# Kernel optimization log

Hardware: AMD Instinct MI355X
Metric: run time of the kernel (lower is better)

The kernel has to match this reference:

```python
import math
import jax, jax.numpy as jnp
import numpy as np

N = 8192
D_IN = 512
D_E = 512


def setup_inputs() -> dict:
    key = jax.random.key(0)
    k1, k2, k3, k4 = jax.random.split(key, 4)
    x = jax.random.normal(k1, (N, D_IN), dtype=jnp.float32)
    A = jax.random.uniform(k2, (N, N), dtype=jnp.float32)
    # xavier-uniform-ish scaling for the two projection weights
    lim_qkv = math.sqrt(6.0 / (D_IN + 3 * D_E))
    Wqkv = jax.random.uniform(k3, (D_IN, 3 * D_E), dtype=jnp.float32, minval=-lim_qkv, maxval=lim_qkv)
    bqkv = jnp.zeros((3 * D_E,), dtype=jnp.float32)
    lim_o = math.sqrt(6.0 / (D_E + D_E))
    Wo = jax.random.uniform(k4, (D_E, D_E), dtype=jnp.float32, minval=-lim_o, maxval=lim_o)
    bo = jnp.zeros((D_E,), dtype=jnp.float32)
    return {"x": x, "A": A, "Wqkv": Wqkv, "bqkv": bqkv, "Wo": Wo, "bo": bo}


def reference(x, A, Wqkv, bqkv, Wo, bo):
    # qkv projection: [N, 3*D_E]
    qkv = x @ Wqkv + bqkv
    q, k, v = jnp.split(qkv, 3, axis=-1)  # each [N, D_E]
    # graph-adjacency transform of keys
    k = A @ k  # [N, D_E]
    scale = 1.0 / math.sqrt(q.shape[-1])
    attn_logits = (q @ k.T) * scale  # [N, N]
    attention = jax.nn.softmax(attn_logits, axis=-1)
    values = attention @ v  # [N, D_E]
    o = values @ Wo + bo
    return (o, attention)
```

## Files before the change

### kernel.cpp

```cpp
#include <hip/hip_runtime.h>

typedef _Float16 half8 __attribute__((ext_vector_type(8)));
typedef _Float16 half4 __attribute__((ext_vector_type(4)));
typedef float f32x4 __attribute__((ext_vector_type(4)));

__global__ __launch_bounds__(256) void transpose_f32(
    const float* __restrict__ in, int lda,
    float* __restrict__ out, int ldo)
{
  __shared__ float t[32][33];
  const int tx = threadIdx.x & 31, ty = threadIdx.x >> 5;
  const int bc = blockIdx.x * 32, br = blockIdx.y * 32;
#pragma unroll
  for (int i = 0; i < 4; ++i)
    t[ty + 8 * i][tx] = in[(size_t)(br + ty + 8 * i) * lda + bc + tx];
  __syncthreads();
#pragma unroll
  for (int i = 0; i < 4; ++i)
    out[(size_t)(bc + ty + 8 * i) * ldo + br + tx] = t[tx][ty + 8 * i];
}

__global__ __launch_bounds__(256) void transpose_f32_f16(
    const float* __restrict__ in, int lda,
    _Float16* __restrict__ out, int ldo)
{
  __shared__ float t[32][33];
  const int tx = threadIdx.x & 31, ty = threadIdx.x >> 5;
  const int bc = blockIdx.x * 32, br = blockIdx.y * 32;
#pragma unroll
  for (int i = 0; i < 4; ++i)
    t[ty + 8 * i][tx] = in[(size_t)(br + ty + 8 * i) * lda + bc + tx];
  __syncthreads();
#pragma unroll
  for (int i = 0; i < 4; ++i)
    out[(size_t)(bc + ty + 8 * i) * ldo + br + tx] = (_Float16)t[tx][ty + 8 * i];
}

__global__ __launch_bounds__(256) void conv_f32_f16(
    const float4* __restrict__ in, _Float16* __restrict__ out)
{
  size_t i = (size_t)blockIdx.x * 256 + threadIdx.x;
  float4 v = in[i];
  half4 h;
  h[0] = (_Float16)v.x; h[1] = (_Float16)v.y;
  h[2] = (_Float16)v.z; h[3] = (_Float16)v.w;
  ((half4*)out)[i] = h;
}

__global__ __launch_bounds__(256) void halfcolsum16(
    const _Float16* __restrict__ k0T16, float* __restrict__ csum)
{
  const int d = blockIdx.x, tid = threadIdx.x;
  float s = 0.f;
#pragma unroll
  for (int i = 0; i < 4; ++i) {
    half8 h = *(const half8*)(k0T16 + (size_t)d * 8192 + i * 2048 + tid * 8);
#pragma unroll
    for (int j = 0; j < 8; ++j) s += (float)h[j];
  }
#pragma unroll
  for (int off = 32; off; off >>= 1) s += __shfl_xor(s, off);
  __shared__ float r[4];
  if ((tid & 63) == 0) r[tid >> 6] = s;
  __syncthreads();
  if (tid == 0) csum[d] = 0.5f * ((r[0] + r[1]) + (r[2] + r[3]));
}

template<int ASPL,int BSPL,int BM,int BN,int WAVES_M,int WAVES_N,int THREADS,
         int APART,bool KSPLIT,bool QF16,int MINW,int AMODE,int BMODE>
__global__ __launch_bounds__(THREADS, MINW) void gemm_bt(
    const void* __restrict__ Agv, int lda, size_t a_plane,
    const void* __restrict__ Bgv, int ldb, size_t b_plane,
    float* __restrict__ Cg, int ldc, size_t c_plane,
    const float* __restrict__ bias, int K, float scale,
    _Float16* __restrict__ q16out)
{
  constexpr int BK = 32;
  constexpr int WM = BM / WAVES_M, WN = BN / WAVES_N;
  constexpr int FM = WM / 16, FN = WN / 16;
  constexpr int NCA = (BM * 4) / THREADS;
  constexpr int NCB = (BN * 4) / THREADS;
  static_assert((BM * 4) % THREADS == 0 && (BN * 4) % THREADS == 0, "mismatch");
  static_assert(AMODE != 3 || ASPL == 1, "AMODE 3 needs ASPL 1");

  __shared__ _Float16 ldsA[2][ASPL][BM][BK];
  __shared__ _Float16 ldsB[2][BSPL][BN][BK];

  const float*    Ag   = (const float*)Agv;
  const _Float16* Ag16 = (const _Float16*)Agv;
  const float*    Bg   = (const float*)Bgv;
  const _Float16* Bg16 = (const _Float16*)Bgv;

  const int tid  = threadIdx.x;
  const int lane = tid & 63;
  const int wid  = tid >> 6;
  const int wrow = wid / WAVES_N, wcol = wid % WAVES_N;
  const int l15  = lane & 15, g = lane >> 4;
  const int brow = blockIdx.y * BM;
  const int bcol = blockIdx.x * BN;

  if constexpr (KSPLIT) {
    const int kc = blockIdx.z;
    Ag += (size_t)kc * K;  Ag16 += (size_t)kc * K;
    Bg += (size_t)kc * K;  Bg16 += (size_t)kc * K;
    Cg += (size_t)kc * c_plane;
  }

  f32x4 acc[FM][FN];
#pragma unroll
  for (int mi = 0; mi < FM; ++mi)
#pragma unroll
    for (int ni = 0; ni < FN; ++ni)
      acc[mi][ni] = (f32x4){0.f, 0.f, 0.f, 0.f};

  float4 ra[NCA][2], rb[NCB][2];
  half8  rah[NCA][2], rbh[NCB][2];

  auto loadAB = [&](int kt) {
    const int k0 = kt * BK;
#pragma unroll
    for (int i = 0; i < NCA; ++i) {
      int c = tid + THREADS * i;
      int row = c >> 2, ci = c & 3;
      if constexpr (AMODE == 3) {
        rah[i][0] = *(const half8*)(Ag16 + (size_t)(brow + row) * lda + k0 + ci * 8);
      } else if constexpr (AMODE == 2) {
        const _Float16* bp = Ag16 + (size_t)(brow + row) * lda + k0 + ci * 8;
        rah[i][0] = *(const half8*)bp;
        rah[i][1] = *(const half8*)(bp + a_plane);
      } else if constexpr (AMODE == 1) {
        float4 u0 = make_float4(0.f, 0.f, 0.f, 0.f);
        float4 u1 = make_float4(0.f, 0.f, 0.f, 0.f);
        const _Float16* bp = Ag16 + (size_t)(brow + row) * lda + k0 + ci * 8;
#pragma unroll
        for (int p = 0; p < APART; ++p) {
          half8 hv = *(const half8*)(bp + (size_t)p * a_plane);
          u0.x += (float)hv[0]; u0.y += (float)hv[1]; u0.z += (float)hv[2]; u0.w += (float)hv[3];
          u1.x += (float)hv[4]; u1.y += (float)hv[5]; u1.z += (float)hv[6]; u1.w += (float)hv[7];
        }
        ra[i][0] = u0; ra[i][1] = u1;
      } else {
        const float* bp = Ag + (size_t)(brow + row) * lda + k0 + ci * 8;
        float4 u0 = ((const float4*)bp)[0];
        float4 u1 = ((const float4*)bp)[1];
#pragma unroll
        for (int p = 1; p < APART; ++p) {
          const float* pp = bp + (size_t)p * a_plane;
          float4 w0 = ((const float4*)pp)[0], w1 = ((const float4*)pp)[1];
          u0.x += w0.x; u0.y += w0.y; u0.z += w0.z; u0.w += w0.w;
          u1.x += w1.x; u1.y += w1.y; u1.z += w1.z; u1.w += w1.w;
        }
        ra[i][0] = u0; ra[i][1] = u1;
      }
    }
#pragma unroll
    for (int i = 0; i < NCB; ++i) {
      int c = tid + THREADS * i;
      int row = c >> 2, ci = c & 3;
      if constexpr (BMODE == 2) {
        const _Float16* bp = Bg16 + (size_t)(bcol + row) * ldb + k0 + ci * 8;
        rbh[i][0] = *(const half8*)bp;
        rbh[i][1] = *(const half8*)(bp + b_plane);
      } else if constexpr (BMODE == 3) {
        rbh[i][0] = *(const half8*)(Bg16 + (size_t)(bcol + row) * ldb + k0 + ci * 8);
      } else {
        const float4* p = (const float4*)(Bg + (size_t)(bcol + row) * ldb + k0 + ci * 8);
        rb[i][0] = p[0]; rb[i][1] = p[1];
      }
    }
  };

  auto stageLDS = [&](int b) {
#pragma unroll
    for (int i = 0; i < NCA; ++i) {
      int c = tid + THREADS * i;
      int row = c >> 2, ci = c & 3;
      int off = row * BK + ((ci ^ ((row >> 1) & 3)) << 3);
      if constexpr (AMODE == 3) {
        *(half8*)(&ldsA[b][0][0][0] + off) = rah[i][0];
      } else if constexpr (AMODE == 2) {
        *(half8*)(&ldsA[b][0][0][0] + off) = rah[i][0];
        *(half8*)(&ldsA[b][1][0][0] + off) = rah[i][1];
      } else {
        float f[8] = {ra[i][0].x, ra[i][0].y, ra[i][0].z, ra[i][0].w,
                      ra[i][1].x, ra[i][1].y, ra[i][1].z, ra[i][1].w};
        half8 h, l;
#pragma unroll
        for (int j = 0; j < 8; ++j) {
          _Float16 hv = (_Float16)f[j];
          h[j] = hv;
          if (ASPL == 2) l[j] = (_Float16)(f[j] - (float)hv);
        }
        *(half8*)(&ldsA[b][0][0][0] + off) = h;
        if (ASPL == 2) *(half8*)(&ldsA[b][1][0][0] + off) = l;
      }
    }
#pragma unroll
    for (int i = 0; i < NCB; ++i) {
      int c = tid + THREADS * i;
      int row = c >> 2, ci = c & 3;
      int off = row * BK + ((ci ^ ((row >> 1) & 3)) << 3);
      if constexpr (BMODE == 2) {
        *(half8*)(&ldsB[b][0][0][0] + off) = rbh[i][0];
        *(half8*)(&ldsB[b][1][0][0] + off) = rbh[i][1];
      } else if constexpr (BMODE == 3) {
        *(half8*)(&ldsB[b][0][0][0] + off) = rbh[i][0];
      } else {
        float f[8] = {rb[i][0].x, rb[i][0].y, rb[i][0].z, rb[i][0].w,
                      rb[i][1].x, rb[i][1].y, rb[i][1].z, rb[i][1].w};
        half8 h, l;
#pragma unroll
        for (int j = 0; j < 8; ++j) {
          _Float16 hv = (_Float16)f[j];
          h[j] = hv;
          if (BSPL == 2) l[j] = (_Float16)(f[j] - (float)hv);
        }
        *(half8*)(&ldsB[b][0][0][0] + off) = h;
        if (BSPL == 2) *(half8*)(&ldsB[b][1][0][0] + off) = l;
      }
    }
  };

  const int nk = K / BK;
  loadAB(0);
  stageLDS(0);
  if (nk > 1) loadAB(1);
  __syncthreads();

  for (int kt = 0; kt < nk; ++kt) {
    const int cur = kt & 1, nxt = cur ^ 1;
    if (kt + 1 < nk) stageLDS(nxt);
    if (kt + 2 < nk) loadAB(kt + 2);

    half8 af[FM][ASPL];
#pragma unroll
    for (int mi = 0; mi < FM; ++mi)
#pragma unroll
      for (int sa = 0; sa < ASPL; ++sa) {
        int row = wrow * WM + mi * 16 + l15;
        af[mi][sa] = *(const half8*)(&ldsA[cur][sa][0][0] + row * BK + ((g ^ ((row >> 1) & 3)) << 3));
      }
#pragma unroll
    for (int ni = 0; ni < FN; ++ni) {
      half8 bf[BSPL];
#pragma unroll
      for (int sb = 0; sb < BSPL; ++sb) {
        int row = wcol * WN + ni * 16 + l15;
        bf[sb] = *(const half8*)(&ldsB[cur][sb][0][0] + row * BK + ((g ^ ((row >> 1) & 3)) << 3));
      }
#pragma unroll
      for (int mi = 0; mi < FM; ++mi)
#pragma unroll
        for (int sa = 0; sa < ASPL; ++sa)
#pragma unroll
          for (int sb = 0; sb < BSPL; ++sb) {
            if (ASPL == 2 && BSPL == 2 && sa == 1 && sb == 1) continue;
            acc[mi][ni] = __builtin_amdgcn_mfma_f32_16x16x32_f16(af[mi][sa], bf[sb], acc[mi][ni], 0, 0, 0);
          }
    }
    __syncthreads();
  }

#pragma unroll
  for (int mi = 0; mi < FM; ++mi)
#pragma unroll
    for (int ni = 0; ni < FN; ++ni) {
      int col = bcol + wcol * WN + ni * 16 + l15;
      float bv = bias ? bias[col] : 0.f;
#pragma unroll
      for (int j = 0; j < 4; ++j) {
        int r = brow + wrow * WM + mi * 16 + g * 4 + j;
        float v = acc[mi][ni][j] * scale + bv;
        if constexpr (QF16) {
          if (col < 512) q16out[(size_t)r * 512 + col] = (_Float16)v;
          else           Cg[(size_t)r * ldc + col] = v;
        } else {
          Cg[(size_t)r * ldc + col] = v;
        }
      }
    }
}

template<int BM,int BN,int THREADS,bool STATS,int MINW>
__global__ __launch_bounds__(THREADS, MINW) void gemm_ff16(
    const _Float16* __restrict__ Ag, int lda,
    const _Float16* __restrict__ Bg, int ldb,
    float* __restrict__ Cg, int ldc,
    int K, float scale,
    float* __restrict__ mxout, float* __restrict__ smout, int ntiles)
{
  constexpr int BK = 32;
  constexpr int WAVES_M = 2, WAVES_N = 2;
  constexpr int WM = BM / WAVES_M, WN = BN / WAVES_N;
  constexpr int FM = WM / 16, FN = WN / 16;
  constexpr int NCA = (BM * 4) / THREADS;
  constexpr int NCB = (BN * 4) / THREADS;

  __shared__ _Float16 ldsA[2][BM][BK];
  __shared__ _Float16 ldsB[2][BN][BK];

  const int tid  = threadIdx.x;
  const int lane = tid & 63;
  const int wid  = tid >> 6;
  const int wrow = wid >> 1, wcol = wid & 1;
  const int l15  = lane & 15, g = lane >> 4;
  const int brow = blockIdx.y * BM;
  const int bcol = blockIdx.x * BN;

  f32x4 acc[FM][FN];
#pragma unroll
  for (int mi = 0; mi < FM; ++mi)
#pragma unroll
    for (int ni = 0; ni < FN; ++ni)
      acc[mi][ni] = (f32x4){0.f, 0.f, 0.f, 0.f};

  half8 ra[NCA], rb[NCB];

  auto loadAB = [&](int kt) {
    const int k0 = kt * BK;
#pragma unroll
    for (int i = 0; i < NCA; ++i) {
      int c = tid + THREADS * i;
      int row = c >> 2, ci = c & 3;
      ra[i] = *(const half8*)(Ag + (size_t)(brow + row) * lda + k0 + ci * 8);
    }
#pragma unroll
    for (int i = 0; i < NCB; ++i) {
      int c = tid + THREADS * i;
      int row = c >> 2, ci = c & 3;
      rb[i] = *(const half8*)(Bg + (size_t)(bcol + row) * ldb + k0 + ci * 8);
    }
  };

  auto stageLDS = [&](int b) {
#pragma unroll
    for (int i = 0; i < NCA; ++i) {
      int c = tid + THREADS * i;
      int row = c >> 2, ci = c & 3;
      int off = row * BK + ((ci ^ ((row >> 1) & 3)) << 3);
      *(half8*)(&ldsA[b][0][0] + off) = ra[i];
    }
#pragma unroll
    for (int i = 0; i < NCB; ++i) {
      int c = tid + THREADS * i;
      int row = c >> 2, ci = c & 3;
      int off = row * BK + ((ci ^ ((row >> 1) & 3)) << 3);
      *(half8*)(&ldsB[b][0][0] + off) = rb[i];
    }
  };

  const int nk = K / BK;
  loadAB(0);
  stageLDS(0);
  if (nk > 1) loadAB(1);
  __syncthreads();

  for (int kt = 0; kt < nk; ++kt) {
    const int cur = kt & 1, nxt = cur ^ 1;
    if (kt + 1 < nk) stageLDS(nxt);
    if (kt + 2 < nk) loadAB(kt + 2);

    half8 af[FM];
#pragma unroll
    for (int mi = 0; mi < FM; ++mi) {
      int row = wrow * WM + mi * 16 + l15;
      af[mi] = *(const half8*)(&ldsA[cur][0][0] + row * BK + ((g ^ ((row >> 1) & 3)) << 3));
    }
#pragma unroll
    for (int ni = 0; ni < FN; ++ni) {
      int row = wcol * WN + ni * 16 + l15;
      half8 bf = *(const half8*)(&ldsB[cur][0][0] + row * BK + ((g ^ ((row >> 1) & 3)) << 3));
#pragma unroll
      for (int mi = 0; mi < FM; ++mi)
        acc[mi][ni] = __builtin_amdgcn_mfma_f32_16x16x32_f16(af[mi], bf, acc[mi][ni], 0, 0, 0);
    }
    __syncthreads();
  }

#pragma unroll
  for (int mi = 0; mi < FM; ++mi)
#pragma unroll
    for (int ni = 0; ni < FN; ++ni) {
      int col = bcol + wcol * WN + ni * 16 + l15;
#pragma unroll
      for (int j = 0; j < 4; ++j) {
        int r = brow + wrow * WM + mi * 16 + g * 4 + j;
        Cg[(size_t)r * ldc + col] = acc[mi][ni][j] * scale;
      }
    }

  if constexpr (STATS) {
    __shared__ float s_m2[BM][2];
    __shared__ float s_s2[BM][2];
#pragma unroll
    for (int mi = 0; mi < FM; ++mi)
#pragma unroll
      for (int j = 0; j < 4; ++j) {
        float v = -3.4e38f;
#pragma unroll
        for (int ni = 0; ni < FN; ++ni) v = fmaxf(v, acc[mi][ni][j] * scale);
        v = fmaxf(v, __shfl_xor(v, 1)); v = fmaxf(v, __shfl_xor(v, 2));
        v = fmaxf(v, __shfl_xor(v, 4)); v = fmaxf(v, __shfl_xor(v, 8));
        if (l15 == 0) s_m2[wrow * WM + mi * 16 + g * 4 + j][wcol] = v;
      }
    __syncthreads();
#pragma unroll
    for (int mi = 0; mi < FM; ++mi)
#pragma unroll
      for (int j = 0; j < 4; ++j) {
        int r = wrow * WM + mi * 16 + g * 4 + j;
        float mt = fmaxf(s_m2[r][0], s_m2[r][1]);
        float s = 0.f;
#pragma unroll
        for (int ni = 0; ni < FN; ++ni) s += __expf(acc[mi][ni][j] * scale - mt);
        s += __shfl_xor(s, 1); s += __shfl_xor(s, 2);
        s += __shfl_xor(s, 4); s += __shfl_xor(s, 8);
        if (l15 == 0) s_s2[r][wcol] = s;
      }
    __syncthreads();
    if (tid < BM) {
      float mt = fmaxf(s_m2[tid][0], s_m2[tid][1]);
      float st = s_s2[tid][0] + s_s2[tid][1];
      mxout[(size_t)(brow + tid) * ntiles + blockIdx.x] = mt;
      smout[(size_t)(brow + tid) * ntiles + blockIdx.x] = st;
    }
  }
}

__global__ __launch_bounds__(256) void reduce4_f16(
    const float4* __restrict__ in, _Float16* __restrict__ out16, size_t plane4,
    const float4* __restrict__ csum4)
{
  size_t i = (size_t)blockIdx.x * 256 + threadIdx.x;
  float4 a = in[i], b = in[plane4 + i], c = in[2 * plane4 + i], d = in[3 * plane4 + i];
  float4 s = csum4[i & 127];
  half4 h;
  h[0] = (_Float16)(a.x + b.x + c.x + d.x - s.x);
  h[1] = (_Float16)(a.y + b.y + c.y + d.y - s.y);
  h[2] = (_Float16)(a.z + b.z + c.z + d.z - s.z);
  h[3] = (_Float16)(a.w + b.w + c.w + d.w - s.w);
  *(half4*)(out16 + i * 4) = h;
}

__global__ __launch_bounds__(256) void softmax_combine(
    const float* __restrict__ mx, const float* __restrict__ sm,
    float* __restrict__ rowm, float* __restrict__ rowinv)
{
  const int row = blockIdx.x * 4 + (threadIdx.x >> 6);
  const int lane = threadIdx.x & 63;
  float mt = mx[(size_t)row * 64 + lane];
  float m = mt;
#pragma unroll
  for (int off = 32; off; off >>= 1) m = fmaxf(m, __shfl_xor(m, off));
  float s = sm[(size_t)row * 64 + lane] * __expf(mt - m);
#pragma unroll
  for (int off = 32; off; off >>= 1) s += __shfl_xor(s, off);
  if (lane == 0) { rowm[row] = m; rowinv[row] = 1.0f / s; }
}

__global__ __launch_bounds__(512, 4) void pv_fused(
    float* __restrict__ attn,
    const _Float16* __restrict__ vT16,
    const float* __restrict__ rowm, const float* __restrict__ rowinv,
    _Float16* __restrict__ vals16)
{
  constexpr int BM = 64, BN = 512, BK = 32, NSTEP = 64;
  __shared__ _Float16 ldsA[2][BM][BK];
  __shared__ _Float16 ldsB[2][BN][BK];
  __shared__ float s_m[BM], s_inv[BM];

  const int tid = threadIdx.x, lane = tid & 63, wid = tid >> 6;
  const int wrow = wid >> 2, wcol = wid & 3;
  const int l15 = lane & 15, g = lane >> 4;
  const int kc = blockIdx.x, brow = blockIdx.y * BM;
  const size_t kbase = (size_t)kc * 2048;

  if (tid < BM) { s_m[tid] = rowm[brow + tid]; s_inv[tid] = rowinv[brow + tid]; }

  f32x4 acc[2][8];
#pragma unroll
  for (int mi = 0; mi < 2; ++mi)
#pragma unroll
    for (int ni = 0; ni < 8; ++ni) acc[mi][ni] = (f32x4){0.f, 0.f, 0.f, 0.f};

  const int arow = (tid & 255) >> 2, aci = tid & 3;
  float4 ra[2];
  half8 rbh[4];

  auto loadA = [&](int kt) {
    if (tid < 256) {
      const float4* p = (const float4*)(attn + (size_t)(brow + arow) * 8192 + kbase + kt * BK + aci * 8);
      ra[0] = p[0]; ra[1] = p[1];
    }
  };
  auto loadB = [&](int kt) {
#pragma unroll
    for (int i = 0; i < 4; ++i) {
      int c = tid + 512 * i; int r = c >> 2, ci = c & 3;
      rbh[i] = *(const half8*)(vT16 + (size_t)r * 8192 + kbase + kt * BK + ci * 8);
    }
  };
  auto stage = [&](int kt, int b) {
    if (tid < 256) {
      const float m = s_m[arow], inv = s_inv[arow];
      float f[8] = {ra[0].x, ra[0].y, ra[0].z, ra[0].w, ra[1].x, ra[1].y, ra[1].z, ra[1].w};
      float e[8]; half8 h;
#pragma unroll
      for (int j = 0; j < 8; ++j) {
        e[j] = __expf(f[j] - m) * inv;
        h[j] = (_Float16)e[j];
      }
      float4* w = (float4*)(attn + (size_t)(brow + arow) * 8192 + kbase + kt * BK + aci * 8);
      w[0] = make_float4(e[0], e[1], e[2], e[3]);
      w[1] = make_float4(e[4], e[5], e[6], e[7]);
      int off = arow * BK + ((aci ^ ((arow >> 1) & 3)) << 3);
      *(half8*)(&ldsA[b][0][0] + off) = h;
    }
#pragma unroll
    for (int i = 0; i < 4; ++i) {
      int c = tid + 512 * i; int r = c >> 2, ci = c & 3;
      int off2 = r * BK + ((ci ^ ((r >> 1) & 3)) << 3);
      *(half8*)(&ldsB[b][0][0] + off2) = rbh[i];
    }
  };

  loadA(0); loadB(0);
  __syncthreads();
  stage(0, 0);
  loadA(1); loadB(1);
  __syncthreads();

  for (int kt = 0; kt < NSTEP; ++kt) {
    const int cur = kt & 1, nxt = cur ^ 1;
    if (kt + 1 < NSTEP) stage(kt + 1, nxt);
    if (kt + 2 < NSTEP) { loadA(kt + 2); loadB(kt + 2); }
    half8 af[2];
#pragma unroll
    for (int mi = 0; mi < 2; ++mi) {
      int row = wrow * 32 + mi * 16 + l15;
      af[mi] = *(const half8*)(&ldsA[cur][0][0] + row * BK + ((g ^ ((row >> 1) & 3)) << 3));
    }
    __builtin_amdgcn_s_setprio(1);
#pragma unroll
    for (int ni = 0; ni < 8; ++ni) {
      int rn = wcol * 128 + ni * 16 + l15;
      half8 bf = *(const half8*)(&ldsB[cur][0][0] + rn * BK + ((g ^ ((rn >> 1) & 3)) << 3));
#pragma unroll
      for (int mi = 0; mi < 2; ++mi)
        acc[mi][ni] = __builtin_amdgcn_mfma_f32_16x16x32_f16(af[mi], bf, acc[mi][ni], 0, 0, 0);
    }
    __builtin_amdgcn_s_setprio(0);
    __syncthreads();
  }

  const size_t plane = (size_t)8192 * 512;
#pragma unroll
  for (int mi = 0; mi < 2; ++mi)
#pragma unroll
    for (int ni = 0; ni < 8; ++ni) {
      int col = wcol * 128 + ni * 16 + l15;
#pragma unroll
      for (int j = 0; j < 4; ++j) {
        int row = brow + wrow * 32 + mi * 16 + g * 4 + j;
        vals16[(size_t)kc * plane + (size_t)row * 512 + col] = (_Float16)acc[mi][ni][j];
      }
    }
}

extern "C" void kernel_launch(void* const* d_in, const int* in_sizes, int n_in,
                              void* d_out, int out_size, void* d_ws, size_t ws_size,
                              hipStream_t stream)
{
  const float* x    = (const float*)d_in[0];
  const float* Amat = (const float*)d_in[1];
  const float* Wqkv = (const float*)d_in[2];
  const float* bqkv = (const float*)d_in[3];
  const float* Wo   = (const float*)d_in[4];
  const float* bo   = (const float*)d_in[5];

  float* o    = (float*)d_out;
  float* attn = (float*)d_out + (size_t)8192 * 512;

  float* ws = (float*)d_ws;
  _Float16*  vals16 = (_Float16*)ws;
  float*     qkv    = ws;
  _Float16*  k0T16  = (_Float16*)(ws + 12582912);
  _Float16*  vT16   = (_Float16*)(ws + 16777216);
  _Float16*  W16T   = (_Float16*)(ws + 18874368);
  float*     WoT    = ws + 19660800;
  _Float16*  kbuf16 = (_Float16*)(ws + 19922944);
  float*     mx     = ws + 24117248;
  float*     sm     = ws + 24641536;
  float*     rowm   = ws + 25165824;
  float*     rowinv = ws + 25174016;
  float*     csum   = ws + 25182208;
  _Float16*  q16    = (_Float16*)(ws + 25183232);
  float*     kpart  = attn;
  _Float16*  x16    = (_Float16*)attn;

  const dim3 b256(256), b512(512);
  const float qk_scale = 0.04419417382415922f;
  const size_t plane = (size_t)8192 * 512;

  conv_f32_f16<<<dim3(4096), b256, 0, stream>>>((const float4*)x, x16);
  transpose_f32_f16<<<dim3(48, 16), b256, 0, stream>>>(Wqkv, 1536, W16T, 512);
  transpose_f32<<<dim3(16, 16), b256, 0, stream>>>(Wo, 512, WoT, 512);

  gemm_bt<1, 1, 128, 128, 2, 2, 256, 1, false, true, 4, 3, 3>
      <<<dim3(12, 64), b256, 0, stream>>>(
      x16, 512, 0, W16T, 512, 0, qkv, 1536, 0, bqkv, 512, 1.0f, q16);

  transpose_f32_f16<<<dim3(16, 256), b256, 0, stream>>>(qkv + 512, 1536, k0T16, 8192);
  transpose_f32_f16<<<dim3(16, 256), b256, 0, stream>>>(qkv + 1024, 1536, vT16, 8192);
  halfcolsum16<<<dim3(512), b256, 0, stream>>>(k0T16, csum);

  gemm_bt<1, 1, 128, 256, 2, 4, 512, 1, true, false, 4, 0, 3>
      <<<dim3(2, 64, 4), b512, 0, stream>>>(
      Amat, 8192, 0, k0T16, 8192, 0, kpart, 512, plane, nullptr, 2048, 1.0f, nullptr);

  reduce4_f16<<<dim3(4096), b256, 0, stream>>>((const float4*)kpart, kbuf16, plane / 4,
                                               (const float4*)csum);

  gemm_ff16<128, 128, 256, true, 4>
      <<<dim3(64, 64), b256, 0, stream>>>(
      q16, 512, kbuf16, 512, attn, 8192, 512, qk_scale, mx, sm, 64);

  softmax_combine<<<dim3(2048), b256, 0, stream>>>(mx, sm, rowm, rowinv);

  pv_fused<<<dim3(4, 128), b512, 0, stream>>>(attn, vT16, rowm, rowinv, vals16);

  gemm_bt<1, 1, 128, 128, 2, 2, 256, 4, false, false, 3, 1, 0>
      <<<dim3(4, 64), b256, 0, stream>>>(
      vals16, 512, plane, WoT, 512, 0, o, 512, 0, bo, 512, 1.0f, nullptr);
}
```

Before: 584.6 us.

## Write QKV projection as fp16, transpose in fp16, and remap QK^T block order

The QKV GEMM now writes its whole output as fp16 into one buffer instead of fp32 qkv plus a separate q16 copy. The K and V transposes read fp16 through a new 64x64 fp16 transpose kernel, and the QK^T GEMM reads q from that buffer with stride 1536. The QK^T kernel also switches to a 1D grid with a workgroup-id remap that interleaves tiles across groups of 8, likely to spread them over XCDs for better L2 locality. This cuts intermediate traffic, but rounding k and v to fp16 before the transpose keeps the same precision as before, and the remap changes which tiles share a cache.

```diff
diff --git a/kernel.cpp b/kernel.cpp
--- a/kernel.cpp
+++ b/kernel.cpp
@@ -34,6 +34,22 @@
 #pragma unroll
   for (int i = 0; i < 4; ++i)
     out[(size_t)(bc + ty + 8 * i) * ldo + br + tx] = (_Float16)t[tx][ty + 8 * i];
+}
+
+__global__ __launch_bounds__(256) void transpose_f16(
+    const _Float16* __restrict__ in, int lda,
+    _Float16* __restrict__ out, int ldo)
+{
+  __shared__ _Float16 t[64][66];
+  const int tx = threadIdx.x & 63, ty = threadIdx.x >> 6;
+  const int bc = blockIdx.x * 64, br = blockIdx.y * 64;
+#pragma unroll
+  for (int i = 0; i < 16; ++i)
+    t[ty + 4 * i][tx] = in[(size_t)(br + ty + 4 * i) * lda + bc + tx];
+  __syncthreads();
+#pragma unroll
+  for (int i = 0; i < 16; ++i)
+    out[(size_t)(bc + ty + 4 * i) * ldo + br + tx] = t[tx][ty + 4 * i];
 }
 
 __global__ __launch_bounds__(256) void conv_f32_f16(
@@ -67,13 +83,13 @@
 }
 
 template<int ASPL,int BSPL,int BM,int BN,int WAVES_M,int WAVES_N,int THREADS,
-         int APART,bool KSPLIT,bool QF16,int MINW,int AMODE,int BMODE>
+         int APART,bool KSPLIT,int CMODE,int MINW,int AMODE,int BMODE>
 __global__ __launch_bounds__(THREADS, MINW) void gemm_bt(
     const void* __restrict__ Agv, int lda, size_t a_plane,
     const void* __restrict__ Bgv, int ldb, size_t b_plane,
     float* __restrict__ Cg, int ldc, size_t c_plane,
     const float* __restrict__ bias, int K, float scale,
-    _Float16* __restrict__ q16out)
+    _Float16* __restrict__ c16out)
 {
   constexpr int BK = 32;
   constexpr int WM = BM / WAVES_M, WN = BN / WAVES_N;
@@ -114,7 +130,7 @@
       acc[mi][ni] = (f32x4){0.f, 0.f, 0.f, 0.f};
 
   float4 ra[NCA][2], rb[NCB][2];
-  half8  rah[NCA][2], rbh[NCB][2];
+  half8  rah[NCA], rbh[NCB];
 
   auto loadAB = [&](int kt) {
     const int k0 = kt * BK;
@@ -123,11 +139,7 @@
       int c = tid + THREADS * i;
       int row = c >> 2, ci = c & 3;
       if constexpr (AMODE == 3) {
-        rah[i][0] = *(const half8*)(Ag16 + (size_t)(brow + row) * lda + k0 + ci * 8);
-      } else if constexpr (AMODE == 2) {
-        const _Float16* bp = Ag16 + (size_t)(brow + row) * lda + k0 + ci * 8;
-        rah[i][0] = *(const half8*)bp;
-        rah[i][1] = *(const half8*)(bp + a_plane);
+        rah[i] = *(const half8*)(Ag16 + (size_t)(brow + row) * lda + k0 + ci * 8);
       } else if constexpr (AMODE == 1) {
         float4 u0 = make_float4(0.f, 0.f, 0.f, 0.f);
         float4 u1 = make_float4(0.f, 0.f, 0.f, 0.f);
@@ -157,12 +169,8 @@
     for (int i = 0; i < NCB; ++i) {
       int c = tid + THREADS * i;
       int row = c >> 2, ci = c & 3;
-      if constexpr (BMODE == 2) {
-        const _Float16* bp = Bg16 + (size_t)(bcol + row) * ldb + k0 + ci * 8;
-        rbh[i][0] = *(const half8*)bp;
-        rbh[i][1] = *(const half8*)(bp + b_plane);
-      } else if constexpr (BMODE == 3) {
-        rbh[i][0] = *(const half8*)(Bg16 + (size_t)(bcol + row) * ldb + k0 + ci * 8);
+      if constexpr (BMODE == 3) {
+        rbh[i] = *(const half8*)(Bg16 + (size_t)(bcol + row) * ldb + k0 + ci * 8);
       } else {
         const float4* p = (const float4*)(Bg + (size_t)(bcol + row) * ldb + k0 + ci * 8);
         rb[i][0] = p[0]; rb[i][1] = p[1];
@@ -177,10 +185,7 @@
       int row = c >> 2, ci = c & 3;
       int off = row * BK + ((ci ^ ((row >> 1) & 3)) << 3);
       if constexpr (AMODE == 3) {
-        *(half8*)(&ldsA[b][0][0][0] + off) = rah[i][0];
-      } else if constexpr (AMODE == 2) {
-        *(half8*)(&ldsA[b][0][0][0] + off) = rah[i][0];
-        *(half8*)(&ldsA[b][1][0][0] + off) = rah[i][1];
+        *(half8*)(&ldsA[b][0][0][0] + off) = rah[i];
       } else {
         float f[8] = {ra[i][0].x, ra[i][0].y, ra[i][0].z, ra[i][0].w,
                       ra[i][1].x, ra[i][1].y, ra[i][1].z, ra[i][1].w};
@@ -200,11 +205,8 @@
       int c = tid + THREADS * i;
       int row = c >> 2, ci = c & 3;
       int off = row * BK + ((ci ^ ((row >> 1) & 3)) << 3);
-      if constexpr (BMODE == 2) {
-        *(half8*)(&ldsB[b][0][0][0] + off) = rbh[i][0];
-        *(half8*)(&ldsB[b][1][0][0] + off) = rbh[i][1];
-      } else if constexpr (BMODE == 3) {
-        *(half8*)(&ldsB[b][0][0][0] + off) = rbh[i][0];
+      if constexpr (BMODE == 3) {
+        *(half8*)(&ldsB[b][0][0][0] + off) = rbh[i];
       } else {
         float f[8] = {rb[i][0].x, rb[i][0].y, rb[i][0].z, rb[i][0].w,
                       rb[i][1].x, rb[i][1].y, rb[i][1].z, rb[i][1].w};
@@ -271,9 +273,8 @@
       for (int j = 0; j < 4; ++j) {
         int r = brow + wrow * WM + mi * 16 + g * 4 + j;
         float v = acc[mi][ni][j] * scale + bv;
-        if constexpr (QF16) {
-          if (col < 512) q16out[(size_t)r * 512 + col] = (_Float16)v;
-          else           Cg[(size_t)r * ldc + col] = v;
+        if constexpr (CMODE == 2) {
+          c16out[(size_t)r * ldc + col] = (_Float16)v;
         } else {
           Cg[(size_t)r * ldc + col] = v;
         }
@@ -304,8 +305,12 @@
   const int wid  = tid >> 6;
   const int wrow = wid >> 1, wcol = wid & 1;
   const int l15  = lane & 15, g = lane >> 4;
-  const int brow = blockIdx.y * BM;
-  const int bcol = blockIdx.x * BN;
+
+  const int id = blockIdx.x;
+  const int wgid = (id & 7) * 512 + (id >> 3);
+  const int bxv = wgid & 63, byv = wgid >> 6;
+  const int brow = byv * BM;
+  const int bcol = bxv * BN;
 
   f32x4 acc[FM][FN];
 #pragma unroll
@@ -421,8 +426,8 @@
     if (tid < BM) {
       float mt = fmaxf(s_m2[tid][0], s_m2[tid][1]);
       float st = s_s2[tid][0] + s_s2[tid][1];
-      mxout[(size_t)(brow + tid) * ntiles + blockIdx.x] = mt;
-      smout[(size_t)(brow + tid) * ntiles + blockIdx.x] = st;
+      mxout[(size_t)(brow + tid) * ntiles + bxv] = mt;
+      smout[(size_t)(brow + tid) * ntiles + bxv] = st;
     }
   }
 }
@@ -583,8 +588,8 @@
 
   float* ws = (float*)d_ws;
   _Float16*  vals16 = (_Float16*)ws;
-  float*     qkv    = ws;
-  _Float16*  k0T16  = (_Float16*)(ws + 12582912);
+  _Float16*  qkv16  = (_Float16*)(ws + 8388608);
+  _Float16*  k0T16  = (_Float16*)(ws + 14680064);
   _Float16*  vT16   = (_Float16*)(ws + 16777216);
   _Float16*  W16T   = (_Float16*)(ws + 18874368);
   float*     WoT    = ws + 19660800;
@@ -594,7 +599,6 @@
   float*     rowm   = ws + 25165824;
   float*     rowinv = ws + 25174016;
   float*     csum   = ws + 25182208;
-  _Float16*  q16    = (_Float16*)(ws + 25183232);
   float*     kpart  = attn;
   _Float16*  x16    = (_Float16*)attn;
 
@@ -606,15 +610,15 @@
   transpose_f32_f16<<<dim3(48, 16), b256, 0, stream>>>(Wqkv, 1536, W16T, 512);
   transpose_f32<<<dim3(16, 16), b256, 0, stream>>>(Wo, 512, WoT, 512);
 
-  gemm_bt<1, 1, 128, 128, 2, 2, 256, 1, false, true, 4, 3, 3>
+  gemm_bt<1, 1, 128, 128, 2, 2, 256, 1, false, 2, 4, 3, 3>
       <<<dim3(12, 64), b256, 0, stream>>>(
-      x16, 512, 0, W16T, 512, 0, qkv, 1536, 0, bqkv, 512, 1.0f, q16);
-
-  transpose_f32_f16<<<dim3(16, 256), b256, 0, stream>>>(qkv + 512, 1536, k0T16, 8192);
-  transpose_f32_f16<<<dim3(16, 256), b256, 0, stream>>>(qkv + 1024, 1536, vT16, 8192);
+      x16, 512, 0, W16T, 512, 0, nullptr, 1536, 0, bqkv, 512, 1.0f, qkv16);
+
+  transpose_f16<<<dim3(8, 128), b256, 0, stream>>>(qkv16 + 512, 1536, k0T16, 8192);
+  transpose_f16<<<dim3(8, 128), b256, 0, stream>>>(qkv16 + 1024, 1536, vT16, 8192);
   halfcolsum16<<<dim3(512), b256, 0, stream>>>(k0T16, csum);
 
-  gemm_bt<1, 1, 128, 256, 2, 4, 512, 1, true, false, 4, 0, 3>
+  gemm_bt<1, 1, 128, 256, 2, 4, 512, 1, true, 0, 4, 0, 3>
       <<<dim3(2, 64, 4), b512, 0, stream>>>(
       Amat, 8192, 0, k0T16, 8192, 0, kpart, 512, plane, nullptr, 2048, 1.0f, nullptr);
 
@@ -622,14 +626,14 @@
                                                (const float4*)csum);
 
   gemm_ff16<128, 128, 256, true, 4>
-      <<<dim3(64, 64), b256, 0, stream>>>(
-      q16, 512, kbuf16, 512, attn, 8192, 512, qk_scale, mx, sm, 64);
+      <<<dim3(4096), b256, 0, stream>>>(
+      qkv16, 1536, kbuf16, 512, attn, 8192, 512, qk_scale, mx, sm, 64);
 
   softmax_combine<<<dim3(2048), b256, 0, stream>>>(mx, sm, rowm, rowinv);
 
   pv_fused<<<dim3(4, 128), b512, 0, stream>>>(attn, vT16, rowm, rowinv, vals16);
 
-  gemm_bt<1, 1, 128, 128, 2, 2, 256, 4, false, false, 3, 1, 0>
+  gemm_bt<1, 1, 128, 128, 2, 2, 256, 4, false, 0, 3, 1, 0>
       <<<dim3(4, 64), b256, 0, stream>>>(
       vals16, 512, plane, WoT, 512, 0, o, 512, 0, bo, 512, 1.0f, nullptr);
 }
```

After: 580.9 us. No clear change (-0.6%).
